# Optimization experiments

Hardware: AMD Instinct MI355X
Metric: run time of the kernel (lower is better)

## Reference

```python
import jax, jax.numpy as jnp
import numpy as np

DEPTH = 2
TWO_PI = 6.283185307179586


def _apply_ry(state, theta, axis):
    """Apply RY(theta) on qubit at `axis` of state [N,2,2,2,2]. theta: [N] or scalar."""
    half = theta * 0.5
    a0 = jnp.take(state, 0, axis=axis)  # [N,2,2,2]
    a1 = jnp.take(state, 1, axis=axis)
    c = jnp.reshape(jnp.cos(half), (-1,) + (1,) * (a0.ndim - 1))
    s = jnp.reshape(jnp.sin(half), (-1,) + (1,) * (a0.ndim - 1))
    return jnp.stack([c * a0 - s * a1, s * a0 + c * a1], axis=axis)


def _apply_cnot(state, c_axis, t_axis):
    a0 = jnp.take(state, 0, axis=c_axis)  # control=0: unchanged
    a1 = jnp.take(state, 1, axis=c_axis)  # control=1: flip target
    t_ax = t_axis - (1 if t_axis > c_axis else 0)
    a1 = jnp.flip(a1, axis=t_ax)
    return jnp.stack([a0, a1], axis=c_axis)


def _simulate(patches, weights):
    """patches: [N,4] angles. Returns <Z_i> for i=0..3, shape [N,4]. All gates real."""
    N = patches.shape[0]
    state = jnp.zeros((N, 2, 2, 2, 2), dtype=patches.dtype)
    state = state.at[:, 0, 0, 0, 0].set(1.0)
    for w in range(4):  # data encoding
        state = _apply_ry(state, patches[:, w], axis=w + 1)
    for d in range(DEPTH):  # variational layers
        for w in range(4):
            state = _apply_ry(state, weights[d, w], axis=w + 1)
        for c, t in ((0, 1), (1, 2), (2, 3)):
            state = _apply_cnot(state, c + 1, t + 1)
    probs = state * state
    zs = []
    for w in range(4):
        p0 = jnp.take(probs, 0, axis=w + 1).sum(axis=(1, 2, 3))
        p1 = jnp.take(probs, 1, axis=w + 1).sum(axis=(1, 2, 3))
        zs.append(p0 - p1)
    return jnp.stack(zs, axis=-1)  # [N,4]


def setup_inputs() -> dict:
    key = jax.random.key(0)
    k1, k2, k3, k4 = jax.random.split(key, 4)
    B = 8192
    x = jax.random.uniform(k1, (B, 1, 28, 28), dtype=jnp.float32)
    weights = jax.random.uniform(k2, (DEPTH, 4), dtype=jnp.float32) * TWO_PI
    W = jax.random.normal(k3, (10, 4 * 14 * 14), dtype=jnp.float32) * 0.02
    b = jax.random.normal(k4, (10,), dtype=jnp.float32) * 0.02
    return {"x": x, "weights": weights, "W": W, "b": b}


def reference(x, weights, W, b):
    B = x.shape[0]
    # Extract non-overlapping 2x2 patches in row-major (i,j) order;
    # within a patch, order is [(i,j),(i,j+1),(i+1,j),(i+1,j+1)] matching x[:,:,i:i+2,j:j+2].view(B,4)
    p = x.reshape(B, 14, 2, 14, 2).transpose(0, 1, 3, 2, 4).reshape(B, 196, 4)
    feats = _simulate(p.reshape(B * 196, 4), weights).reshape(B, 196 * 4)
    logits = feats @ W.T + b
    return jax.nn.log_softmax(logits, axis=-1)
```

## Files before the change

kernel.cpp:

```cpp
#include <hip/hip_runtime.h>
#include <math.h>

#define IMGS 4

__device__ __forceinline__ float rfl(float v) {
    return __int_as_float(__builtin_amdgcn_readfirstlane(__float_as_int(v)));
}

__global__ __launch_bounds__(256, 8) void quanv_kernel(
    const float* __restrict__ x,
    const float* __restrict__ wts,
    const float* __restrict__ W,
    const float* __restrict__ bias,
    float* __restrict__ out,
    int B)
{
    __shared__ __align__(16) float feats[IMGS][788];
    __shared__ float part[4][IMGS][10];
    __shared__ float logits[IMGS][10];
    __shared__ float lsev[IMGS];

    const int tid  = threadIdx.x;
    const int img0 = blockIdx.x * IMGS;
    constexpr float inv2pi = 0.15915494309189535f;

    float cw1[4], sw1[4], w0r[4];
#pragma unroll
    for (int q = 0; q < 4; ++q) {
        w0r[q] = rfl(wts[q] * inv2pi);
        float r = wts[4 + q] * inv2pi;
        r -= floorf(r);
        cw1[q] = __builtin_amdgcn_cosf(r);
        sw1[q] = __builtin_amdgcn_sinf(r);
    }
    const float cc  = cw1[0]*cw1[1], cs = cw1[0]*sw1[1];
    const float sc  = sw1[0]*cw1[1], ss = sw1[0]*sw1[1];
    const float ccc = cc*cw1[2], ccs = cc*sw1[2], csc = cs*cw1[2], css = cs*sw1[2];
    const float scc = sc*cw1[2], ssc = ss*cw1[2], sss = ss*sw1[2];
    const float K0 = rfl(cw1[0]),       K1 = rfl(-sw1[0]);
    const float K2 = rfl(cc),           K3 = rfl(-cs),          K4 = rfl(ss);
    const float K5 = rfl(ccc),          K6 = rfl(-ccs),         K7 = rfl(css);
    const float K8 = rfl(-scc),         K9 = rfl(-sss);
    const float L1 = rfl(ccc*cw1[3]),   L2 = rfl(-ccc*sw1[3]);
    const float L3 = rfl(ccs*sw1[3]),   L4 = rfl(-csc*cw1[3]);
    const float L5 = rfl(-css*sw1[3]),  L6 = rfl(scc*sw1[3]);
    const float L7 = rfl(ssc*cw1[3]),   L8 = rfl(sss*sw1[3]);

#pragma unroll
    for (int it = 0; it < 4; ++it) {
        const int p = tid + it * 256;
        const int img = p / 196;
        const int pl  = p - img * 196;
        if (p < IMGS * 196 && img0 + img < B) {
            const int pi = pl / 14, pj = pl - pi * 14;
            const float* xp = x + (size_t)(img0 + img) * 784 + pi * 56 + pj * 2;
            const float2 t0 = *(const float2*)xp;
            const float2 t1 = *(const float2*)(xp + 28);

            float r;
            r = fmaf(t0.x, inv2pi, w0r[0]); r -= floorf(r);
            const float a  = __builtin_amdgcn_sinf(r), A  = __builtin_amdgcn_cosf(r);
            r = fmaf(t0.y, inv2pi, w0r[1]); r -= floorf(r);
            const float b  = __builtin_amdgcn_sinf(r), Bv = __builtin_amdgcn_cosf(r);
            r = fmaf(t1.x, inv2pi, w0r[2]); r -= floorf(r);
            const float c  = __builtin_amdgcn_sinf(r), C  = __builtin_amdgcn_cosf(r);
            r = fmaf(t1.y, inv2pi, w0r[3]); r -= floorf(r);
            const float d  = __builtin_amdgcn_sinf(r), D  = __builtin_amdgcn_cosf(r);

            const float ab=a*b, bc=b*c, ac=a*c, cd=c*d, bd=b*d, ad=a*d;
            const float AC=A*C, Ab=A*b, Bc=Bv*c, BD=Bv*D, cD=c*D, Cd=C*d;

            const float z0 = fmaf(K0, A,  K1*ab);
            const float z1 = fmaf(K2, Bv, fmaf(K3, A*bc, K4*ac));
            const float z2 = fmaf(K5, AC, fmaf(K6, Bv*cd,
                             fmaf(K7, A*bd, fmaf(K8, ab*C, K9*ad))));
            const float z3 = fmaf(L1, BD, fmaf(L2, AC*d, fmaf(L3, Bc,
                             fmaf(L4, Ab*cD, fmaf(L5, Ab, fmaf(L6, ab*Cd,
                             fmaf(L7, ac*D, L8*a)))))));

            *(float4*)&feats[img][pl * 4] = make_float4(z0, z1, z2, z3);
        }
    }
    __syncthreads();

    const int wave = tid >> 6, lane = tid & 63;
    const int img  = lane & 3, sub = lane >> 2;
    const int slot = wave * 16 + sub;

    float acc[10];
#pragma unroll
    for (int cl = 0; cl < 10; ++cl) acc[cl] = 0.f;

#pragma unroll
    for (int it = 0; it < 4; ++it) {
        const int g = it * 64 + slot;
        if (g < 196) {
            const float4 f = *(const float4*)&feats[img][g * 4];
#pragma unroll
            for (int cl = 0; cl < 10; ++cl) {
                const float4 wv = *(const float4*)&W[cl * 784 + g * 4];
                acc[cl] = fmaf(f.x, wv.x, fmaf(f.y, wv.y,
                          fmaf(f.z, wv.z, fmaf(f.w, wv.w, acc[cl]))));
            }
        }
    }
#pragma unroll
    for (int cl = 0; cl < 10; ++cl) {
        acc[cl] += __shfl_xor(acc[cl], 4, 64);
        acc[cl] += __shfl_xor(acc[cl], 8, 64);
        acc[cl] += __shfl_xor(acc[cl], 16, 64);
        acc[cl] += __shfl_xor(acc[cl], 32, 64);
    }
    if (lane < IMGS) {
#pragma unroll
        for (int cl = 0; cl < 10; ++cl) part[wave][lane][cl] = acc[cl];
    }
    __syncthreads();

    if (tid < IMGS * 10) {
        const int im = tid / 10, cl = tid - (tid / 10) * 10;
        logits[im][cl] = bias[cl] + part[0][im][cl] + part[1][im][cl]
                       + part[2][im][cl] + part[3][im][cl];
    }
    __syncthreads();
    if (tid < IMGS) {
        float m = -1e30f;
#pragma unroll
        for (int j = 0; j < 10; ++j) m = fmaxf(m, logits[tid][j]);
        float s = 0.f;
#pragma unroll
        for (int j = 0; j < 10; ++j) s += __expf(logits[tid][j] - m);
        lsev[tid] = m + __logf(s);
    }
    __syncthreads();
    if (tid < IMGS * 10) {
        const int im = tid / 10, cl = tid - (tid / 10) * 10;
        if (img0 + im < B)
            out[(size_t)(img0 + im) * 10 + cl] = logits[im][cl] - lsev[im];
    }
}

extern "C" void kernel_launch(void* const* d_in, const int* in_sizes, int n_in,
                              void* d_out, int out_size, void* d_ws, size_t ws_size,
                              hipStream_t stream) {
    const float* x    = (const float*)d_in[0];
    const float* wts  = (const float*)d_in[1];
    const float* W    = (const float*)d_in[2];
    const float* bias = (const float*)d_in[3];
    float* out        = (float*)d_out;

    const int B = in_sizes[0] / 784;
    const int blocks = (B + IMGS - 1) / IMGS;
    quanv_kernel<<<blocks, 256, 0, stream>>>(x, wts, W, bias, out, B);
}
```

Measured before the change: 22.25 us.

## Map one image per wavefront and fuse feature compute into the GEMV without LDS

Each wavefront now handles a whole image: lanes compute patch features and multiply them directly against W in registers. This removes the shared-memory feature buffer, the block barriers and the cross-wave partial reduction, and log-softmax is done redundantly in every lane. The costs are that input loads are less coalesced across images, W is read per wave with a different access pattern, and the launch-bounds occupancy hint is dropped.

After: 19.26 us. -13.4%, faster.

```diff
diff --git a/kernel.cpp b/kernel.cpp
--- a/kernel.cpp
+++ b/kernel.cpp
@@ -1,13 +1,13 @@
 #include <hip/hip_runtime.h>
 #include <math.h>
 
-#define IMGS 4
+#define INV2PI 0.15915494309189535f
 
 __device__ __forceinline__ float rfl(float v) {
     return __int_as_float(__builtin_amdgcn_readfirstlane(__float_as_int(v)));
 }
 
-__global__ __launch_bounds__(256, 8) void quanv_kernel(
+__global__ __launch_bounds__(256) void quanv_wave_kernel(
     const float* __restrict__ x,
     const float* __restrict__ wts,
     const float* __restrict__ W,
@@ -15,20 +15,15 @@
     float* __restrict__ out,
     int B)
 {
-    __shared__ __align__(16) float feats[IMGS][788];
-    __shared__ float part[4][IMGS][10];
-    __shared__ float logits[IMGS][10];
-    __shared__ float lsev[IMGS];
+    const int lane = threadIdx.x & 63;
+    const int img  = blockIdx.x * 4 + (threadIdx.x >> 6);
+    if (img >= B) return;
 
-    const int tid  = threadIdx.x;
-    const int img0 = blockIdx.x * IMGS;
-    constexpr float inv2pi = 0.15915494309189535f;
-
-    float cw1[4], sw1[4], w0r[4];
+    float w0r[4], cw1[4], sw1[4];
 #pragma unroll
     for (int q = 0; q < 4; ++q) {
-        w0r[q] = rfl(wts[q] * inv2pi);
-        float r = wts[4 + q] * inv2pi;
+        w0r[q] = rfl(wts[q] * INV2PI);
+        float r = wts[4 + q] * INV2PI;
         r -= floorf(r);
         cw1[q] = __builtin_amdgcn_cosf(r);
         sw1[q] = __builtin_amdgcn_sinf(r);
@@ -46,25 +41,29 @@
     const float L5 = rfl(-css*sw1[3]),  L6 = rfl(scc*sw1[3]);
     const float L7 = rfl(ssc*cw1[3]),   L8 = rfl(sss*sw1[3]);
 
+    const float* xim = x + (size_t)img * 784;
+
+    float acc[10];
 #pragma unroll
-    for (int it = 0; it < 4; ++it) {
-        const int p = tid + it * 256;
-        const int img = p / 196;
-        const int pl  = p - img * 196;
-        if (p < IMGS * 196 && img0 + img < B) {
-            const int pi = pl / 14, pj = pl - pi * 14;
-            const float* xp = x + (size_t)(img0 + img) * 784 + pi * 56 + pj * 2;
+    for (int cl = 0; cl < 10; ++cl) acc[cl] = 0.f;
+
+#pragma unroll
+    for (int i = 0; i < 4; ++i) {
+        const int p = i * 64 + lane;
+        if (p < 196) {
+            const int pi = p / 14, pj = p - pi * 14;
+            const float* xp = xim + pi * 56 + pj * 2;
             const float2 t0 = *(const float2*)xp;
             const float2 t1 = *(const float2*)(xp + 28);
 
             float r;
-            r = fmaf(t0.x, inv2pi, w0r[0]); r -= floorf(r);
+            r = fmaf(t0.x, INV2PI, w0r[0]); r -= floorf(r);
             const float a  = __builtin_amdgcn_sinf(r), A  = __builtin_amdgcn_cosf(r);
-            r = fmaf(t0.y, inv2pi, w0r[1]); r -= floorf(r);
+            r = fmaf(t0.y, INV2PI, w0r[1]); r -= floorf(r);
             const float b  = __builtin_amdgcn_sinf(r), Bv = __builtin_amdgcn_cosf(r);
-            r = fmaf(t1.x, inv2pi, w0r[2]); r -= floorf(r);
+            r = fmaf(t1.x, INV2PI, w0r[2]); r -= floorf(r);
             const float c  = __builtin_amdgcn_sinf(r), C  = __builtin_amdgcn_cosf(r);
-            r = fmaf(t1.y, inv2pi, w0r[3]); r -= floorf(r);
+            r = fmaf(t1.y, INV2PI, w0r[3]); r -= floorf(r);
             const float d  = __builtin_amdgcn_sinf(r), D  = __builtin_amdgcn_cosf(r);
 
             const float ab=a*b, bc=b*c, ac=a*c, cd=c*d, bd=b*d, ad=a*d;
@@ -78,65 +77,42 @@
                              fmaf(L4, Ab*cD, fmaf(L5, Ab, fmaf(L6, ab*Cd,
                              fmaf(L7, ac*D, L8*a)))))));
 
-            *(float4*)&feats[img][pl * 4] = make_float4(z0, z1, z2, z3);
-        }
-    }
-    __syncthreads();
-
-    const int wave = tid >> 6, lane = tid & 63;
-    const int img  = lane & 3, sub = lane >> 2;
-    const int slot = wave * 16 + sub;
-
-    float acc[10];
-#pragma unroll
-    for (int cl = 0; cl < 10; ++cl) acc[cl] = 0.f;
-
-#pragma unroll
-    for (int it = 0; it < 4; ++it) {
-        const int g = it * 64 + slot;
-        if (g < 196) {
-            const float4 f = *(const float4*)&feats[img][g * 4];
+            const float* wp = W + p * 4;
 #pragma unroll
             for (int cl = 0; cl < 10; ++cl) {
-                const float4 wv = *(const float4*)&W[cl * 784 + g * 4];
-                acc[cl] = fmaf(f.x, wv.x, fmaf(f.y, wv.y,
-                          fmaf(f.z, wv.z, fmaf(f.w, wv.w, acc[cl]))));
+                const float4 wv = *(const float4*)(wp + cl * 784);
+                acc[cl] = fmaf(z0, wv.x, fmaf(z1, wv.y,
+                          fmaf(z2, wv.z, fmaf(z3, wv.w, acc[cl]))));
             }
         }
     }
+
 #pragma unroll
     for (int cl = 0; cl < 10; ++cl) {
+        acc[cl] += __shfl_xor(acc[cl], 1, 64);
+        acc[cl] += __shfl_xor(acc[cl], 2, 64);
         acc[cl] += __shfl_xor(acc[cl], 4, 64);
         acc[cl] += __shfl_xor(acc[cl], 8, 64);
         acc[cl] += __shfl_xor(acc[cl], 16, 64);
         acc[cl] += __shfl_xor(acc[cl], 32, 64);
+        acc[cl] += bias[cl];
     }
-    if (lane < IMGS) {
+
+    float m = acc[0];
 #pragma unroll
-        for (int cl = 0; cl < 10; ++cl) part[wave][lane][cl] = acc[cl];
-    }
-    __syncthreads();
+    for (int cl = 1; cl < 10; ++cl) m = fmaxf(m, acc[cl]);
+    float s = 0.f;
+#pragma unroll
+    for (int cl = 0; cl < 10; ++cl) s += __expf(acc[cl] - m);
+    const float lse = m + __logf(s);
 
-    if (tid < IMGS * 10) {
-        const int im = tid / 10, cl = tid - (tid / 10) * 10;
-        logits[im][cl] = bias[cl] + part[0][im][cl] + part[1][im][cl]
-                       + part[2][im][cl] + part[3][im][cl];
-    }
-    __syncthreads();
-    if (tid < IMGS) {
-        float m = -1e30f;
-#pragma unroll
-        for (int j = 0; j < 10; ++j) m = fmaxf(m, logits[tid][j]);
-        float s = 0.f;
-#pragma unroll
-        for (int j = 0; j < 10; ++j) s += __expf(logits[tid][j] - m);
-        lsev[tid] = m + __logf(s);
-    }
-    __syncthreads();
-    if (tid < IMGS * 10) {
-        const int im = tid / 10, cl = tid - (tid / 10) * 10;
-        if (img0 + im < B)
-            out[(size_t)(img0 + im) * 10 + cl] = logits[im][cl] - lsev[im];
+    if (lane == 0) {
+        float* op = out + (size_t)img * 10;
+        *(float2*)(op + 0) = make_float2(acc[0] - lse, acc[1] - lse);
+        *(float2*)(op + 2) = make_float2(acc[2] - lse, acc[3] - lse);
+        *(float2*)(op + 4) = make_float2(acc[4] - lse, acc[5] - lse);
+        *(float2*)(op + 6) = make_float2(acc[6] - lse, acc[7] - lse);
+        *(float2*)(op + 8) = make_float2(acc[8] - lse, acc[9] - lse);
     }
 }
 
@@ -150,6 +126,6 @@
     float* out        = (float*)d_out;
 
     const int B = in_sizes[0] / 784;
-    const int blocks = (B + IMGS - 1) / IMGS;
-    quanv_kernel<<<blocks, 256, 0, stream>>>(x, wts, W, bias, out, B);
+    const int blocks = (B + 3) / 4;
+    quanv_wave_kernel<<<blocks, 256, 0, stream>>>(x, wts, W, bias, out, B);
 }
```
